# Performance work log

Hardware: AMD Instinct MI355X
Metric: run time of the kernel (lower is better)

## Reference

```python
import jax, jax.numpy as jnp
import numpy as np

D_MODEL, D_QKV, N_HEADS = 1024, 64, 16


def setup_inputs() -> dict:
    key = jax.random.key(0)
    k_x, k_qkv, k_out = jax.random.split(key, 3)
    X = jax.random.normal(k_x, (2, 2048, D_MODEL), dtype=jnp.float32)
    # nn.Linear(d_model, 3*d_qkv*n_heads, bias=False): store as (in, out) for X @ W
    W_qkv = jax.random.normal(k_qkv, (D_MODEL, 3 * D_QKV * N_HEADS), dtype=jnp.float32) * (D_MODEL ** -0.5)
    W_out = jax.random.normal(k_out, (D_QKV * N_HEADS, D_MODEL), dtype=jnp.float32) * ((D_QKV * N_HEADS) ** -0.5)
    return {"X": X, "W_qkv": W_qkv, "W_out": W_out}


def reference(X, W_qkv, W_out):
    b, s, _ = X.shape
    h, d = N_HEADS, D_QKV
    scale = d ** 0.5
    qkv = X @ W_qkv                          # [b, s, 3*h*d]
    # Faithful to torch: view(b, s, h, d, 3).unbind(-1) -> interleaved q/k/v layout
    qkv = qkv.reshape(b, s, h, d, 3)
    q, k, v = qkv[..., 0], qkv[..., 1], qkv[..., 2]   # each [b, s, h, d]
    scores = jnp.einsum("bqhd,bkhd->bhqk", q, k) / scale
    weights = jax.nn.softmax(scores, axis=-1)          # [b, h, s, s]
    attn = jnp.einsum("bhqk,bkhd->bqhd", weights, v)   # [b, s, h, d]
    return attn.reshape(b, s, h * d) @ W_out           # [b, s, d_model]
```

## Files before the change

### kernel.cpp

```cpp
#include <hip/hip_runtime.h>
#include <hip/hip_bf16.h>
#include <math.h>

typedef __bf16 bf16;
typedef __bf16 bf16x2 __attribute__((ext_vector_type(2)));
typedef __bf16 bf16x4 __attribute__((ext_vector_type(4)));
typedef __bf16 bf16x8 __attribute__((ext_vector_type(8)));
typedef float f32x2 __attribute__((ext_vector_type(2)));
typedef float f32x4 __attribute__((ext_vector_type(4)));
typedef float f32x16 __attribute__((ext_vector_type(16)));
typedef int i32x2 __attribute__((ext_vector_type(2)));
typedef int i32x4 __attribute__((ext_vector_type(4)));

#define MFMA16(a, b, c) __builtin_amdgcn_mfma_f32_16x16x32_bf16(a, b, c, 0, 0, 0)
#define MFMA32(a, b, c) __builtin_amdgcn_mfma_f32_32x32x16_bf16(a, b, c, 0, 0, 0)

constexpr int D_MODEL = 1024;
constexpr int N_QKV   = 3072;
constexpr int BATCH   = 2;
constexpr int SEQ     = 2048;
constexpr int NH      = 16;
constexpr int DH      = 64;
constexpr int M_TOT   = BATCH * SEQ;

__device__ __forceinline__ void gl_lds16(const bf16* g, bf16* l) {
    __builtin_amdgcn_global_load_lds(
        (const __attribute__((address_space(1))) void*)g,
        (__attribute__((address_space(3))) void*)l, 16, 0, 0);
}

__device__ __forceinline__ void pl32swap(int& a, int& b) {
    i32x2 r = __builtin_amdgcn_permlane32_swap(a, b, false, false);
    a = r[0];
    b = r[1];
}

template <int N> __device__ __forceinline__ void waitv() {
    asm volatile("s_waitcnt vmcnt(%0)" :: "n"(N) : "memory");
}

__device__ __forceinline__ void transpose_tile(
    const float* __restrict__ in, bf16* __restrict__ out,
    int K, int N, int n0, int k0, bf16 (*T)[72], bool permute)
{
    const int tid = threadIdx.x;
    const int r   = tid >> 2;
    const int c4  = (tid & 3) * 16;

    const float* src = in + (size_t)(k0 + r) * N + n0 + c4;
    f32x4 v0 = *(const f32x4*)(src + 0);
    f32x4 v1 = *(const f32x4*)(src + 4);
    f32x4 v2 = *(const f32x4*)(src + 8);
    f32x4 v3 = *(const f32x4*)(src + 12);
    #pragma unroll
    for (int j = 0; j < 4; j++) {
        T[c4 + j][r]      = (bf16)v0[j];
        T[c4 + 4 + j][r]  = (bf16)v1[j];
        T[c4 + 8 + j][r]  = (bf16)v2[j];
        T[c4 + 12 + j][r] = (bf16)v3[j];
    }
    __syncthreads();
    int rowg = n0 + r;
    if (permute) {
        const int which = rowg % 3;
        const int h     = rowg / 192;
        const int d     = (rowg % 192) / 3;
        rowg = which * 1024 + h * 64 + d;
    }
    bf16* dst = out + (size_t)rowg * K + k0 + c4;
    *(bf16x8*)(dst)     = *(const bf16x8*)&T[r][c4];
    *(bf16x8*)(dst + 8) = *(const bf16x8*)&T[r][c4 + 8];
}

__global__ __launch_bounds__(256) void prepass_kernel(
    const float* __restrict__ X, const float* __restrict__ Wqkv,
    const float* __restrict__ Wout,
    bf16* __restrict__ xb, bf16* __restrict__ wqkv_t, bf16* __restrict__ wout_t)
{
    __shared__ bf16 T[64][72];
    const int b = blockIdx.x;
    if (b < 2048) {
        const size_t i = ((size_t)b * 256 + threadIdx.x) * 8;
        f32x4 a0 = *(const f32x4*)(X + i);
        f32x4 a1 = *(const f32x4*)(X + i + 4);
        bf16x8 w;
        #pragma unroll
        for (int j = 0; j < 4; j++) { w[j] = (bf16)a0[j]; w[j + 4] = (bf16)a1[j]; }
        *(bf16x8*)(xb + i) = w;
    } else if (b < 2048 + 768) {
        const int idx = b - 2048;
        transpose_tile(Wqkv, wqkv_t, D_MODEL, N_QKV,
                       (idx % 48) * 64, (idx / 48) * 64, T, true);
    } else {
        const int idx = b - 2816;
        transpose_tile(Wout, wout_t, D_MODEL, D_MODEL,
                       (idx % 16) * 64, (idx / 16) * 64, T, false);
    }
}

__global__ __launch_bounds__(512, 2) void qkv_gemm_kernel(
    const bf16* __restrict__ Xb, const bf16* __restrict__ Wt,
    bf16* __restrict__ qb, bf16* __restrict__ kb, bf16* __restrict__ vb)
{
    __shared__ __align__(16) bf16 smem[65536];
    bf16* const sA = smem;
    bf16* const sB = smem + 32768;

    const int tid  = threadIdx.x;
    const int wave = tid >> 6;
    const int lane = tid & 63;
    const int quad = lane >> 4;
    const int l16  = lane & 15;
    const int wr   = wave >> 2;
    const int wc   = wave & 3;
    const int m0   = blockIdx.x * 256;
    const int n0   = blockIdx.y * 256;

    const int sr2  = tid >> 3;
    const int c8p  = (tid & 7) ^ (sr2 & 7);
    const int stR0 = (sr2 << 1) | (c8p >> 2);
    const int stC0 = (c8p & 3) << 3;

    const bf16* Asrc = Xb + (size_t)(m0 + stR0) * D_MODEL + stC0;
    const bf16* Bsrc = Wt + (size_t)(n0 + stR0) * D_MODEL + stC0;

#define STG(s, kbo)                                                          \
    do {                                                                     \
        gl_lds16(Asrc + (kbo),                 sA + (s) * 8192 + tid * 8);   \
        gl_lds16(Asrc + 128 * D_MODEL + (kbo), sA + (s) * 8192 + 4096 + tid * 8); \
        gl_lds16(Bsrc + (kbo),                 sB + (s) * 8192 + tid * 8);   \
        gl_lds16(Bsrc + 128 * D_MODEL + (kbo), sB + (s) * 8192 + 4096 + tid * 8); \
    } while (0)

    const int foff = ((l16 >> 1) << 6) +
                     (((((l16 & 1) << 2) | quad) ^ ((l16 >> 1) & 7)) << 3);

    f32x4 acc[8][4];
    #pragma unroll
    for (int a = 0; a < 8; a++)
        #pragma unroll
        for (int b = 0; b < 4; b++) acc[a][b] = {0.f, 0.f, 0.f, 0.f};

    bf16x8 afA[8], bfA[4], afB[8], bfB[4];

    STG(0, 0); STG(1, 32); STG(2, 64);
    waitv<4>();
    __builtin_amdgcn_s_barrier();
    {
        const bf16* A0 = sA + wr * 4096;
        const bf16* B0 = sB + wc * 2048;
        #pragma unroll
        for (int mi = 0; mi < 8; mi++)
            afA[mi] = *(const bf16x8*)&A0[mi * 512 + foff];
        #pragma unroll
        for (int ni = 0; ni < 4; ni++)
            bfA[ni] = *(const bf16x8*)&B0[ni * 512 + foff];
    }

    int p = 0;

#define PHASE(CA, CB, NA, NB, DOSTG, DONXT, WV)                              \
    {                                                                        \
        if (DOSTG) { const int kst = p + 3; STG((kst & 3), kst * 32); }      \
        const int sn = (p + 1) & 3;                                          \
        const bf16* An_ = sA + sn * 8192 + wr * 4096;                        \
        const bf16* Bn_ = sB + sn * 8192 + wc * 2048;                        \
        __builtin_amdgcn_s_setprio(1);                                       \
        _Pragma("unroll") for (int c = 0; c < 4; c++) {                      \
            _Pragma("unroll") for (int m2 = 0; m2 < 2; m2++)                 \
                _Pragma("unroll") for (int ni = 0; ni < 4; ni++)             \
                    acc[c * 2 + m2][ni] =                                    \
                        MFMA16(CA[c * 2 + m2], CB[ni], acc[c * 2 + m2][ni]); \
            if (DONXT) {                                                     \
                NA[c * 2]     = *(const bf16x8*)&An_[(c * 2) * 512 + foff];  \
                NA[c * 2 + 1] = *(const bf16x8*)&An_[(c * 2 + 1) * 512 + foff]; \
            }                                                                \
        }                                                                    \
        if (DONXT) {                                                         \
            _Pragma("unroll") for (int ni = 0; ni < 4; ni++)                 \
                NB[ni] = *(const bf16x8*)&Bn_[ni * 512 + foff];              \
        }                                                                    \
        __builtin_amdgcn_s_setprio(0);                                       \
        waitv<WV>();                                                         \
        __builtin_amdgcn_s_barrier();                                        \
        ++p;                                                                 \
    }

    for (int t = 0; t < 14; ++t) {
        PHASE(afA, bfA, afB, bfB, true, true, 4)
        PHASE(afB, bfB, afA, bfA, true, true, 4)
    }
    PHASE(afA, bfA, afB, bfB, true,  true,  4)
    PHASE(afB, bfB, afA, bfA, false, true,  0)
    PHASE(afA, bfA, afB, bfB, false, true,  0)
    PHASE(afB, bfB, afA, bfA, false, false, 0)

#undef PHASE
#undef STG

    const int bb     = m0 >> 11;
    const int s_base = m0 & (SEQ - 1);

    if (n0 < 2048) {
        bf16* dst0 = (n0 < 1024) ? qb : kb;
        const int h = ((n0 + wc * 64) >> 6) & 15;
        const size_t bh = (size_t)(bb * NH + h);
        #pragma unroll
        for (int mi = 0; mi < 8; mi++) {
            const int s0 = s_base + wr * 128 + mi * 16 + quad * 4;
            #pragma unroll
            for (int ni = 0; ni < 4; ni++) {
                const int d = ni * 16 + l16;
                #pragma unroll
                for (int i = 0; i < 4; i++)
                    dst0[(bh * SEQ + s0 + i) * DH + d] = (bf16)acc[mi][ni][i];
            }
        }
    } else {
        __syncthreads();
        bf16* T = smem;
        #pragma unroll
        for (int ni = 0; ni < 4; ni++) {
            const int nl = wc * 64 + ni * 16 + l16;
            #pragma unroll
            for (int mi = 0; mi < 8; mi++) {
                const int ml = wr * 128 + mi * 16 + quad * 4;
                bf16x4 pv;
                #pragma unroll
                for (int i = 0; i < 4; i++) pv[i] = (bf16)acc[mi][ni][i];
                const int c   = ml >> 3;
                const int swz = (c & 24) | ((c ^ nl) & 7);
                *(bf16x4*)&T[nl * 256 + swz * 8 + (ml & 7)] = pv;
            }
        }
        __syncthreads();
        const int hbase = (n0 - 2048) >> 6;
        #pragma unroll
        for (int it = 0; it < 8; it++) {
            const int nl = (tid >> 4) + it * 32;
            const int h  = hbase + (nl >> 6);
            const int d  = nl & 63;
            const size_t obase = ((size_t)(bb * NH + h) * DH + d) * SEQ + s_base;
            #pragma unroll
            for (int cc = 0; cc < 2; cc++) {
                const int c   = (tid & 15) + cc * 16;
                const int swz = (c & 24) | ((c ^ nl) & 7);
                bf16x8 vv = *(const bf16x8*)&T[nl * 256 + swz * 8];
                *(bf16x8*)(vb + obase + c * 8) = vv;
            }
        }
    }
}

__global__ __launch_bounds__(512, 4) void attn_kernel(
    const bf16* __restrict__ qb, const bf16* __restrict__ kb,
    const bf16* __restrict__ vb, bf16* __restrict__ ob)
{
    __shared__ __align__(16) bf16 smem[32768];

    const int tid  = threadIdx.x;
    const int wave = tid >> 6;
    const int grp  = wave >> 2;
    const int wq   = wave & 3;
    const int lane = tid & 63;
    const int l32  = lane & 31;
    const int hi   = lane >> 5;
    const int ltid = tid & 255;
    const int bh   = blockIdx.x;
    const int q0   = blockIdx.y * 128;
    const size_t base  = (size_t)bh * SEQ * DH;
    const int    kbase = grp * (SEQ / 2);

    bf16* const KsB = smem + grp * 2 * 4096;
    bf16* const VtB = smem + 16384 + grp * 2 * 4096;

    constexpr float QSCALE = 0.125f * 1.44269504f;

    bf16x8 qf[4];
    {
        const size_t qoff = base + (size_t)(q0 + wq * 32 + l32) * DH + hi * 8;
        #pragma unroll
        for (int kc = 0; kc < 4; kc++) {
            qf[kc] = *(const bf16x8*)(qb + qoff + kc * 16);
            #pragma unroll
            for (int j = 0; j < 8; j++)
                qf[kc][j] = (bf16)((float)qf[kc][j] * QSCALE);
        }
    }

    f32x16 o_acc[2];
    #pragma unroll
    for (int i = 0; i < 16; i++) { o_acc[0][i] = 0.f; o_acc[1][i] = 0.f; }
    float l_acc = 0.f;

    const int swz = (l32 & 7) ^ (l32 >> 3);

    const int so0 = ltid;
    const int so1 = 256 + ltid;
    const int sr0 = so0 >> 3, sc0 = ((so0 & 7) ^ (sr0 & 7) ^ ((sr0 >> 3) & 3)) * 8;
    const int sr1 = so1 >> 3, sc1 = ((so1 & 7) ^ (sr1 & 7) ^ ((sr1 >> 3) & 3)) * 8;

    #define STAGE(bufi, kk0)                                                   \
        do {                                                                   \
            gl_lds16(kb + base + (size_t)(kbase + (kk0) + sr0) * DH + sc0,     \
                     KsB + (bufi) * 4096 + so0 * 8);                           \
            gl_lds16(kb + base + (size_t)(kbase + (kk0) + sr1) * DH + sc1,     \
                     KsB + (bufi) * 4096 + so1 * 8);                           \
            gl_lds16(vb + base + (size_t)sr0 * SEQ + kbase + (kk0) + sc0,      \
                     VtB + (bufi) * 4096 + so0 * 8);                           \
            gl_lds16(vb + base + (size_t)sr1 * SEQ + kbase + (kk0) + sc1,      \
                     VtB + (bufi) * 4096 + so1 * 8);                           \
        } while (0)

    STAGE(0, 0);
    int buf = 0;

    for (int kt = 0; kt < SEQ / 128; ++kt) {
        __syncthreads();
        if (kt + 1 < SEQ / 128) STAGE(buf ^ 1, (kt + 1) * 64);

        const bf16* Kst = KsB + buf * 4096;
        const bf16* Vtt = VtB + buf * 4096;

        #pragma unroll
        for (int kblk = 0; kblk < 2; kblk++) {
            f32x16 sacc;
            #pragma unroll
            for (int i = 0; i < 16; i++) sacc[i] = 0.f;
            #pragma unroll
            for (int kc = 0; kc < 4; kc++) {
                const int cko = ((2 * kc + hi) ^ swz) * 8;
                bf16x8 kf = *(const bf16x8*)
                    &Kst[(kblk * 32 + l32) * 64 + cko];
                sacc = MFMA32(kf, qf[kc], sacc);
            }

            int w[8];
            #pragma unroll
            for (int c = 0; c < 8; c++) {
                const float e0 = __builtin_amdgcn_exp2f(sacc[2 * c]);
                const float e1 = __builtin_amdgcn_exp2f(sacc[2 * c + 1]);
                l_acc += e0;
                l_acc += e1;
                bf16x2 t; t[0] = (bf16)e0; t[1] = (bf16)e1;
                w[c] = __builtin_bit_cast(int, t);
            }
            #pragma unroll
            for (int cc = 0; cc < 2; cc++) {
                pl32swap(w[cc * 4 + 0], w[cc * 4 + 2]);
                pl32swap(w[cc * 4 + 1], w[cc * 4 + 3]);
                i32x4 fi = {w[cc * 4 + 0], w[cc * 4 + 1],
                            w[cc * 4 + 2], w[cc * 4 + 3]};
                bf16x8 pa = __builtin_bit_cast(bf16x8, fi);

                const int kc = kblk * 2 + cc;
                const int cko = ((2 * kc + hi) ^ swz) * 8;
                #pragma unroll
                for (int nb = 0; nb < 2; nb++) {
                    bf16x8 vf = *(const bf16x8*)
                        &Vtt[(nb * 32 + l32) * 64 + cko];
                    o_acc[nb] = MFMA32(pa, vf, o_acc[nb]);
                }
            }
        }
        buf ^= 1;
    }
    #undef STAGE

    const float l_q = l_acc + __shfl_xor(l_acc, 32);

    float* cO  = (float*)smem;
    float* cL1 = (float*)smem + 8192;
    float* cL2 = (float*)smem + 8320;

    __syncthreads();
    if (grp == 1) {
        #pragma unroll
        for (int nb = 0; nb < 2; nb++)
            #pragma unroll
            for (int c4 = 0; c4 < 4; c4++) {
                const int j = nb * 4 + c4;
                f32x4 v = { o_acc[nb][c4 * 4 + 0], o_acc[nb][c4 * 4 + 1],
                            o_acc[nb][c4 * 4 + 2], o_acc[nb][c4 * 4 + 3] };
                *(f32x4*)&cO[(wq * 64 + lane) * 32 + ((j ^ (lane & 7)) * 4)] = v;
            }
        if (hi == 0) cL1[wq * 32 + l32] = l_q;
    }
    __syncthreads();
    if (grp == 0) {
        #pragma unroll
        for (int nb = 0; nb < 2; nb++)
            #pragma unroll
            for (int c4 = 0; c4 < 4; c4++) {
                const int j = nb * 4 + c4;
                f32x4 v = *(const f32x4*)
                    &cO[(wq * 64 + lane) * 32 + ((j ^ (lane & 7)) * 4)];
                #pragma unroll
                for (int e = 0; e < 4; e++) o_acc[nb][c4 * 4 + e] += v[e];
            }
        if (hi == 0) cL2[wq * 32 + l32] = l_q + cL1[wq * 32 + l32];
    }
    __syncthreads();
    if (grp == 0) {
        const int b = bh >> 4, h = bh & 15;
        #pragma unroll
        for (int i = 0; i < 16; i++) {
            const int qrow = (i & 3) + 8 * (i >> 2) + 4 * hi;
            const int q = q0 + wq * 32 + qrow;
            const float li = 1.0f / cL2[wq * 32 + qrow];
            #pragma unroll
            for (int nb = 0; nb < 2; nb++)
                ob[((size_t)(b * SEQ + q) * NH + h) * DH + nb * 32 + l32] =
                    (bf16)(o_acc[nb][i] * li);
        }
    }
}

__global__ __launch_bounds__(256, 2) void out_gemm_kernel(
    const bf16* __restrict__ A, const bf16* __restrict__ Wt,
    float* __restrict__ out)
{
    __shared__ __align__(16) bf16 smem[32768];
    bf16* const sA = smem;
    bf16* const sB = smem + 16384;

    const int tid  = threadIdx.x;
    const int wave = tid >> 6;
    const int lane = tid & 63;
    const int quad = lane >> 4;
    const int l16  = lane & 15;
    const int wr   = wave >> 1;
    const int wc   = wave & 1;
    const int m0   = blockIdx.x * 128;
    const int n0   = blockIdx.y * 128;

    const int sr2  = tid >> 3;
    const int c8p  = (tid & 7) ^ (sr2 & 7);
    const int stR0 = (sr2 << 1) | (c8p >> 2);
    const int stC0 = (c8p & 3) << 3;

    const bf16* Asrc = A  + (size_t)(m0 + stR0) * D_MODEL + stC0;
    const bf16* Bsrc = Wt + (size_t)(n0 + stR0) * D_MODEL + stC0;

#define STG(s, kbo)                                                          \
    do {                                                                     \
        gl_lds16(Asrc + (kbo),                sA + (s) * 4096 + tid * 8);    \
        gl_lds16(Asrc + 64 * D_MODEL + (kbo), sA + (s) * 4096 + 2048 + tid * 8); \
        gl_lds16(Bsrc + (kbo),                sB + (s) * 4096 + tid * 8);    \
        gl_lds16(Bsrc + 64 * D_MODEL + (kbo), sB + (s) * 4096 + 2048 + tid * 8); \
    } while (0)

    const int foff = ((l16 >> 1) << 6) +
                     (((((l16 & 1) << 2) | quad) ^ ((l16 >> 1) & 7)) << 3);

    f32x4 acc[4][4];
    #pragma unroll
    for (int a = 0; a < 4; a++)
        #pragma unroll
        for (int b = 0; b < 4; b++) acc[a][b] = {0.f, 0.f, 0.f, 0.f};

    bf16x8 afA[4], bfA[4], afB[4], bfB[4];

    STG(0, 0); STG(1, 32); STG(2, 64);
    waitv<4>();
    __builtin_amdgcn_s_barrier();
    {
        const bf16* A0 = sA + wr * 2048;
        const bf16* B0 = sB + wc * 2048;
        #pragma unroll
        for (int mi = 0; mi < 4; mi++)
            afA[mi] = *(const bf16x8*)&A0[mi * 512 + foff];
        #pragma unroll
        for (int ni = 0; ni < 4; ni++)
            bfA[ni] = *(const bf16x8*)&B0[ni * 512 + foff];
    }

    int p = 0;

#define PHASE(CA, CB, NA, NB, DOSTG, DONXT, WV)                              \
    {                                                                        \
        if (DOSTG) { const int kst = p + 3; STG((kst & 3), kst * 32); }      \
        const int sn = (p + 1) & 3;                                          \
        const bf16* An_ = sA + sn * 4096 + wr * 2048;                        \
        const bf16* Bn_ = sB + sn * 4096 + wc * 2048;                        \
        __builtin_amdgcn_s_setprio(1);                                       \
        _Pragma("unroll") for (int mi = 0; mi < 4; mi++) {                   \
            _Pragma("unroll") for (int ni = 0; ni < 4; ni++)                 \
                acc[mi][ni] = MFMA16(CA[mi], CB[ni], acc[mi][ni]);           \
            if (DONXT) NA[mi] = *(const bf16x8*)&An_[mi * 512 + foff];       \
        }                                                                    \
        if (DONXT) {                                                         \
            _Pragma("unroll") for (int ni = 0; ni < 4; ni++)                 \
                NB[ni] = *(const bf16x8*)&Bn_[ni * 512 + foff];              \
        }                                                                    \
        __builtin_amdgcn_s_setprio(0);                                       \
        waitv<WV>();                                                         \
        __builtin_amdgcn_s_barrier();                                        \
        ++p;                                                                 \
    }

    for (int t = 0; t < 14; ++t) {
        PHASE(afA, bfA, afB, bfB, true, true, 4)
        PHASE(afB, bfB, afA, bfA, true, true, 4)
    }
    PHASE(afA, bfA, afB, bfB, true,  true,  4)
    PHASE(afB, bfB, afA, bfA, false, true,  0)
    PHASE(afA, bfA, afB, bfB, false, true,  0)
    PHASE(afB, bfB, afA, bfA, false, false, 0)

#undef PHASE
#undef STG

    #pragma unroll
    for (int mi = 0; mi < 4; mi++) {
        const int row0 = m0 + wr * 64 + mi * 16 + quad * 4;
        #pragma unroll
        for (int ni = 0; ni < 4; ni++) {
            const int n = n0 + wc * 64 + ni * 16 + l16;
            #pragma unroll
            for (int i = 0; i < 4; i++)
                out[(size_t)(row0 + i) * D_MODEL + n] = acc[mi][ni][i];
        }
    }
}

extern "C" void kernel_launch(void* const* d_in, const int* in_sizes, int n_in,
                              void* d_out, int out_size, void* d_ws, size_t ws_size,
                              hipStream_t stream)
{
    const float* X    = (const float*)d_in[0];
    const float* Wqkv = (const float*)d_in[1];
    const float* Wout = (const float*)d_in[2];
    float* out        = (float*)d_out;

    const size_t n_elem = (size_t)M_TOT * D_MODEL;
    bf16* qb      = (bf16*)d_ws;
    bf16* kb      = qb + n_elem;
    bf16* vb      = kb + n_elem;
    bf16* attnb   = vb + n_elem;
    bf16* wqkv_t  = attnb + n_elem;
    bf16* wout_t  = wqkv_t + (size_t)N_QKV * D_MODEL;
    bf16* xb      = wout_t + (size_t)D_MODEL * D_MODEL;

    prepass_kernel<<<3072, 256, 0, stream>>>(X, Wqkv, Wout, xb, wqkv_t, wout_t);

    qkv_gemm_kernel<<<dim3(M_TOT / 256, N_QKV / 256), 512, 0, stream>>>(
        xb, wqkv_t, qb, kb, vb);
    attn_kernel<<<dim3(BATCH * NH, SEQ / 128), 512, 0, stream>>>(qb, kb, vb, attnb);
    out_gemm_kernel<<<dim3(M_TOT / 128, D_MODEL / 128), 256, 0, stream>>>(
        attnb, wout_t, out);
}
```

Before: 160.4 us.

## Restructure QKV GEMM mainloop into double-buffered K=64 tiles with quarter-phase staging

Rewrites the QKV projection GEMM main loop. It now uses two LDS buffers of K=64 tiles instead of four K=32 stages, and splits each tile into four quarter phases. Each phase issues global-to-LDS loads for the next tiles, reads only the A fragments it needs (B fragments once per tile), and runs MFMAs between barriers. The aim is finer interleaving of loads, LDS reads and MFMAs with fewer register-held fragments and fewer iterations. In exchange it adds two barriers per quarter, an lgkmcnt wait before compute, and a new swizzle pattern that must stay conflict-free and correct.

```diff
diff --git a/kernel.cpp b/kernel.cpp
--- a/kernel.cpp
+++ b/kernel.cpp
@@ -116,24 +116,32 @@
     const int m0   = blockIdx.x * 256;
     const int n0   = blockIdx.y * 256;
 
-    const int sr2  = tid >> 3;
-    const int c8p  = (tid & 7) ^ (sr2 & 7);
-    const int stR0 = (sr2 << 1) | (c8p >> 2);
-    const int stC0 = (c8p & 3) << 3;
-
-    const bf16* Asrc = Xb + (size_t)(m0 + stR0) * D_MODEL + stC0;
-    const bf16* Bsrc = Wt + (size_t)(n0 + stR0) * D_MODEL + stC0;
-
-#define STG(s, kbo)                                                          \
-    do {                                                                     \
-        gl_lds16(Asrc + (kbo),                 sA + (s) * 8192 + tid * 8);   \
-        gl_lds16(Asrc + 128 * D_MODEL + (kbo), sA + (s) * 8192 + 4096 + tid * 8); \
-        gl_lds16(Bsrc + (kbo),                 sB + (s) * 8192 + tid * 8);   \
-        gl_lds16(Bsrc + 128 * D_MODEL + (kbo), sB + (s) * 8192 + 4096 + tid * 8); \
+    const int rA = tid >> 3;
+    const int cA = ((tid & 7) ^ (rA & 7)) * 8;
+    const bf16* Asrc = Xb + (size_t)(m0 + rA) * D_MODEL + cA;
+    const bf16* Bsrc = Wt + (size_t)(n0 + rA) * D_MODEL + cA;
+
+#define STG_B(d_, h, kt) do {                                                \
+        gl_lds16(Bsrc + (size_t)((h) * 128     ) * D_MODEL + (kt) * 64,      \
+                 sB + (d_) * 16384 + (h) * 8192 + tid * 8);                  \
+        gl_lds16(Bsrc + (size_t)((h) * 128 + 64) * D_MODEL + (kt) * 64,      \
+                 sB + (d_) * 16384 + (h) * 8192 + 4096 + tid * 8);           \
     } while (0)
-
-    const int foff = ((l16 >> 1) << 6) +
-                     (((((l16 & 1) << 2) | quad) ^ ((l16 >> 1) & 7)) << 3);
+#define STG_A01(d_, kt) do {                                                 \
+        gl_lds16(Asrc                         + (kt) * 64,                   \
+                 sA + (d_) * 16384 +        tid * 8);                        \
+        gl_lds16(Asrc + (size_t)128 * D_MODEL + (kt) * 64,                   \
+                 sA + (d_) * 16384 + 8192 + tid * 8);                        \
+    } while (0)
+#define STG_A23(d_, kt) do {                                                 \
+        gl_lds16(Asrc + (size_t) 64 * D_MODEL + (kt) * 64,                   \
+                 sA + (d_) * 16384 + 4096        + tid * 8);                 \
+        gl_lds16(Asrc + (size_t)192 * D_MODEL + (kt) * 64,                   \
+                 sA + (d_) * 16384 + 8192 + 4096 + tid * 8);                 \
+    } while (0)
+
+    const int co0 = ((quad    ) ^ (l16 & 7)) * 8;
+    const int co1 = ((quad + 4) ^ (l16 & 7)) * 8;
 
     f32x4 acc[8][4];
     #pragma unroll
@@ -141,62 +149,59 @@
         #pragma unroll
         for (int b = 0; b < 4; b++) acc[a][b] = {0.f, 0.f, 0.f, 0.f};
 
-    bf16x8 afA[8], bfA[4], afB[8], bfB[4];
-
-    STG(0, 0); STG(1, 32); STG(2, 64);
-    waitv<4>();
+    STG_A01(0, 0); STG_A23(0, 0); STG_B(0, 0, 0); STG_B(0, 1, 0);
+    STG_A01(1, 1); STG_A23(1, 1); STG_B(1, 0, 1); STG_B(1, 1, 1);
+    waitv<8>();
     __builtin_amdgcn_s_barrier();
-    {
-        const bf16* A0 = sA + wr * 4096;
-        const bf16* B0 = sB + wc * 2048;
-        #pragma unroll
-        for (int mi = 0; mi < 8; mi++)
-            afA[mi] = *(const bf16x8*)&A0[mi * 512 + foff];
-        #pragma unroll
-        for (int ni = 0; ni < 4; ni++)
-            bfA[ni] = *(const bf16x8*)&B0[ni * 512 + foff];
-    }
-
-    int p = 0;
-
-#define PHASE(CA, CB, NA, NB, DOSTG, DONXT, WV)                              \
+
+#define QPH(Q, CERT6, CERT0, ...)                                            \
     {                                                                        \
-        if (DOSTG) { const int kst = p + 3; STG((kst & 3), kst * 32); }      \
-        const int sn = (p + 1) & 3;                                          \
-        const bf16* An_ = sA + sn * 8192 + wr * 4096;                        \
-        const bf16* Bn_ = sB + sn * 8192 + wc * 2048;                        \
-        __builtin_amdgcn_s_setprio(1);                                       \
-        _Pragma("unroll") for (int c = 0; c < 4; c++) {                      \
-            _Pragma("unroll") for (int m2 = 0; m2 < 2; m2++)                 \
-                _Pragma("unroll") for (int ni = 0; ni < 4; ni++)             \
-                    acc[c * 2 + m2][ni] =                                    \
-                        MFMA16(CA[c * 2 + m2], CB[ni], acc[c * 2 + m2][ni]); \
-            if (DONXT) {                                                     \
-                NA[c * 2]     = *(const bf16x8*)&An_[(c * 2) * 512 + foff];  \
-                NA[c * 2 + 1] = *(const bf16x8*)&An_[(c * 2 + 1) * 512 + foff]; \
+        if ((Q) == 0) {                                                      \
+            _Pragma("unroll") for (int ni = 0; ni < 4; ni++) {               \
+                bfr[ni][0] = *(const bf16x8*)&Bb_[(ni * 16 + l16) * 64 + co0]; \
+                bfr[ni][1] = *(const bf16x8*)&Bb_[(ni * 16 + l16) * 64 + co1]; \
             }                                                                \
         }                                                                    \
-        if (DONXT) {                                                         \
-            _Pragma("unroll") for (int ni = 0; ni < 4; ni++)                 \
-                NB[ni] = *(const bf16x8*)&Bn_[ni * 512 + foff];              \
+        bf16x8 af[2][2];                                                     \
+        _Pragma("unroll") for (int m2 = 0; m2 < 2; m2++) {                   \
+            af[m2][0] = *(const bf16x8*)&Ab_[(((Q)*2+m2)*16 + l16)*64 + co0];\
+            af[m2][1] = *(const bf16x8*)&Ab_[(((Q)*2+m2)*16 + l16)*64 + co1];\
         }                                                                    \
+        __VA_ARGS__;                                                         \
+        __builtin_amdgcn_s_barrier();                                        \
+        asm volatile("s_waitcnt lgkmcnt(0)" ::: "memory");                   \
+        __builtin_amdgcn_s_setprio(1);                                       \
+        _Pragma("unroll") for (int m2 = 0; m2 < 2; m2++)                     \
+            _Pragma("unroll") for (int ni = 0; ni < 4; ni++) {               \
+                acc[(Q)*2+m2][ni] =                                          \
+                    MFMA16(af[m2][0], bfr[ni][0], acc[(Q)*2+m2][ni]);        \
+                acc[(Q)*2+m2][ni] =                                          \
+                    MFMA16(af[m2][1], bfr[ni][1], acc[(Q)*2+m2][ni]);        \
+            }                                                                \
         __builtin_amdgcn_s_setprio(0);                                       \
-        waitv<WV>();                                                         \
+        if (CERT6) { waitv<6>(); } else if (CERT0) { waitv<0>(); }           \
         __builtin_amdgcn_s_barrier();                                        \
-        ++p;                                                                 \
-    }
-
-    for (int t = 0; t < 14; ++t) {
-        PHASE(afA, bfA, afB, bfB, true, true, 4)
-        PHASE(afB, bfB, afA, bfA, true, true, 4)
-    }
-    PHASE(afA, bfA, afB, bfB, true,  true,  4)
-    PHASE(afB, bfB, afA, bfA, false, true,  0)
-    PHASE(afA, bfA, afB, bfB, false, true,  0)
-    PHASE(afB, bfB, afA, bfA, false, false, 0)
-
-#undef PHASE
-#undef STG
+    }
+
+    for (int g = 0; g < 16; ++g) {
+        const int d = g & 1;
+        const bf16* Ab_ = sA + d * 16384 + wr * 8192;
+        const bf16* Bb_ = sB + d * 16384 + (wc >> 1) * 8192 + (wc & 1) * 4096;
+        const bool sm = (g <= 13);
+        const bool sp = (g >= 1 && g <= 14);
+
+        bf16x8 bfr[4][2];
+
+        QPH(0, false, false, if (sp) STG_A23(d ^ 1, g + 1))
+        QPH(1, false, false, if (sm) STG_B(d, 0, g + 2))
+        QPH(2, false, false, if (sm) STG_B(d, 1, g + 2))
+        QPH(3, (g < 14), (g >= 14), if (sm) STG_A01(d, g + 2))
+    }
+
+#undef QPH
+#undef STG_A23
+#undef STG_A01
+#undef STG_B
 
     const int bb     = m0 >> 11;
     const int s_base = m0 & (SEQ - 1);
```

New measurement: 166.9 us. 1.04x slower.
